# Optimization experiments

Hardware: AMD Instinct MI355X
Metric: run time of the kernel (lower is better)

The kernel has to match this reference:

```python
import jax, jax.numpy as jnp
import numpy as np

B = 32768
PASSES = 4

# mask layout: (batch, digit, row, col), values in {0,1}

def _to_lines(m, d):
    """Reorder so the last axis enumerates the 9 cells of a line and axis -2 the 9 lines."""
    if d == 'h':
        return m                      # lines = rows, cells = cols
    if d == 'v':
        return jnp.swapaxes(m, 2, 3)  # lines = cols, cells = rows
    b = m.shape[0]                    # lines = 3x3 boxes
    return m.reshape(b, 9, 3, 3, 3, 3).transpose(0, 1, 2, 4, 3, 5).reshape(b, 9, 9, 9)

_from_lines = _to_lines  # all three reorderings are self-inverse


def filter_line(m, d):
    """SudokuFilterHVBox: remove a solved cell's digit from all other cells in its line."""
    l = _to_lines(m, d)
    cnt = l.sum(axis=1, keepdims=True)                 # candidates per cell
    solved = l * (cnt == 1).astype(l.dtype)            # one-hot solved cells
    other = solved.sum(axis=-1, keepdims=True) - solved  # same digit solved elsewhere in line
    out = l * (other == 0).astype(l.dtype)
    return _from_lines(out, d)


def unique_line(m, d):
    """SudokuUniqueHVBox (hidden single): if a digit fits only one cell in a line, fix it."""
    l = _to_lines(m, d)
    cnt_line = l.sum(axis=-1, keepdims=True)           # per-digit count in the line
    hidden = l * (cnt_line == 1).astype(l.dtype)       # lone placements
    has = hidden.sum(axis=1, keepdims=True) > 0        # cell hosts a hidden single
    out = jnp.where(has, hidden, l)
    return _from_lines(out, d)


def doubles_line(m, d):
    """SudokuDigitsDoubles (naked pair): two identical 2-candidate cells in a line
    eliminate those digits from the rest of the line."""
    l = _to_lines(m, d)                                # (B, d, line, cell)
    cnt = l.sum(axis=1, keepdims=True)
    pm = l * (cnt == 2).astype(l.dtype)                # patterns of 2-candidate cells
    dot = jnp.einsum('bdlc,bdle->blce', pm, pm)        # pattern overlap between cells
    eye = jnp.eye(9, dtype=l.dtype)
    match = (dot == 2).astype(l.dtype) * (1.0 - eye)   # identical pair at another cell
    pairflag = match.sum(-1) > 0                       # (B, line, cell) part of a naked pair
    pair_digit = pm * pairflag[:, None, :, :].astype(l.dtype)
    total_pd = pair_digit.sum(-1, keepdims=True)       # digit belongs to some pair in line
    remove = (total_pd > 0) & (pair_digit == 0)
    out = l * (1.0 - remove.astype(l.dtype))
    return _from_lines(out, d)


def pointing(m, d):
    """SudokuDigitsInOneLineAtBox: if a digit's box candidates lie in one row/col,
    remove that digit from the rest of the row/col outside the box."""
    b = m.shape[0]
    v = m.reshape(b, 9, 3, 3, 3, 3)                    # (B, d, br, ri, bc, ci)
    if d == 'h':
        pres = v.sum(axis=5) > 0                       # (B,d,br,ri,bc) digit in row of box
        nrows = pres.sum(axis=3, keepdims=True)
        point = pres & (nrows == 1)                    # confined to single row within box
        tot = point.sum(axis=4, keepdims=True)         # over bc
        rem = (tot - point) > 0                        # pointing from another box hits us
        out = v * (1.0 - rem[..., None].astype(v.dtype))
    else:
        pres = v.sum(axis=3) > 0                       # (B,d,br,bc,ci) digit in col of box
        ncols = pres.sum(axis=4, keepdims=True)
        point = pres & (ncols == 1)
        tot = point.sum(axis=2, keepdims=True)         # over br
        rem = (tot - point) > 0
        out = v * (1.0 - rem[:, :, :, None, :, :].astype(v.dtype))
    return out.reshape(b, 9, 9, 9)


def _forward_mask(mask):
    for _ in range(PASSES):
        mask = filter_line(mask, 'box')
        mask = pointing(mask, 'h')
        mask = pointing(mask, 'v')
        mask = unique_line(mask, 'h')
        mask = unique_line(mask, 'v')
        mask = unique_line(mask, 'box')
        mask = doubles_line(mask, 'v')   # original code instantiates doubles_h with 'v'
        mask = doubles_line(mask, 'v')
        mask = doubles_line(mask, 'box')
    return mask


def setup_inputs() -> dict:
    key = jax.random.key(0)
    mask = jax.random.randint(key, (B, 9, 9, 9), 0, 2).astype(jnp.float32)
    return {"mask": mask}


def reference(mask):
    out = _forward_mask(mask)
    cnt = out.sum(axis=1)                              # candidates per cell
    solved = jnp.all(cnt == 1, axis=(1, 2))            # (B,) puzzle fully determined
    return (out, solved)
```

## Files before the change

### kernel.cpp

```cpp
#include <hip/hip_runtime.h>
#include <stdint.h>

#define NB 32768
#define NPASS 4
#define FULL27 0x07FFFFFFu
#define PUZ_PER_BLK 64
#define SOLVE_BLKS (NB / PUZ_PER_BLK)
#define BLK_DW 1458
#define BLK_V4 11664


__device__ __forceinline__ uint32_t colfold(uint32_t w) {
    return (w | (w >> 9) | (w >> 18)) & 0x1FFu;
}
__device__ __forceinline__ uint32_t colmaj2(uint32_t w) {
    return ((w & (w >> 9)) | ((w | (w >> 9)) & (w >> 18))) & 0x1FFu;
}
__device__ __forceinline__ uint32_t rotA(uint32_t v) {
    return (uint32_t)__builtin_amdgcn_update_dpp(0, (int)v, 0x09, 0xF, 0xF, true);
}
__device__ __forceinline__ uint32_t rotB(uint32_t v) {
    return (uint32_t)__builtin_amdgcn_update_dpp(0, (int)v, 0x12, 0xF, 0xF, true);
}
__device__ __forceinline__ uint32_t dppx1(uint32_t v) {
    return (uint32_t)__builtin_amdgcn_update_dpp(0, (int)v, 0xB1, 0xF, 0xF, true);
}
__device__ __forceinline__ uint32_t dppx2(uint32_t v) {
    return (uint32_t)__builtin_amdgcn_update_dpp(0, (int)v, 0x4E, 0xF, 0xF, true);
}

__global__ __launch_bounds__(256)
void sudoku_kernel(const uint32_t* __restrict__ in, float* __restrict__ out,
                   float* __restrict__ solved) {
    __shared__ uint32_t pool[BLK_DW + 2];
    const int tid = threadIdx.x;
    const int q = tid >> 2;
    const int band = tid & 3;
    const int P0 = blockIdx.x * PUZ_PER_BLK;

    {
        const uint4* src = (const uint4*)in + (size_t)blockIdx.x * BLK_V4;
        uint16_t* hp = (uint16_t*)pool;
        #pragma unroll 1
        for (int ii = 0; ii < 6; ++ii) {
            uint4 v[8];
            #pragma unroll
            for (int j = 0; j < 8; ++j) {
                int vi = (ii * 8 + j) * 256 + tid;
                if (vi > BLK_V4 - 1) vi = BLK_V4 - 1;
                v[j] = src[vi];
            }
            #pragma unroll
            for (int j = 0; j < 8; ++j) {
                int it = ii * 8 + j;
                uint32_t n = ((v[j].x >> 23) & 1u) | ((v[j].y >> 22) & 2u)
                           | ((v[j].z >> 21) & 4u) | ((v[j].w >> 20) & 8u);
                uint32_t b = n | (dppx1(n) << 4);
                uint32_t h = b | (dppx2(b) << 8);
                if ((tid & 3) == 0) {
                    int D = it * 32 + (tid >> 3);
                    if (D < BLK_DW)
                        hp[2 * D + ((tid >> 2) & 1)] = (uint16_t)h;
                }
            }
        }
    }
    __syncthreads();

    uint32_t bd[9];
    {
        const int bb0 = q * 729 + band * 27;
        #pragma unroll
        for (int d = 0; d < 9; ++d) {
            int bit = bb0 + d * 81;
            int di = bit >> 5, sh = bit & 31;
            uint64_t both = (uint64_t)pool[di] | ((uint64_t)pool[di + 1] << 32);
            bd[d] = (uint32_t)(both >> sh) & FULL27;
        }
    }
    __syncthreads();

    #pragma unroll 1
    for (int pass = 0; pass < NPASS; ++pass) {
        {
            uint32_t on = 0, tw = 0, fo = 0;
            #pragma unroll
            for (int d = 0; d < 9; ++d) {
                uint32_t c = on & bd[d];
                on ^= bd[d]; fo |= tw & c; tw ^= c;
            }
            uint32_t ex1 = on & ~tw & ~fo;
            #pragma unroll
            for (int d = 0; d < 9; ++d) {
                uint32_t s = bd[d] & ex1;
                #pragma unroll
                for (int k = 0; k < 3; ++k) {
                    uint32_t bm = 0x1C0E07u << (3 * k);
                    uint32_t sm = s & bm;
                    uint32_t multi = sm & (sm - 1u);
                    uint32_t keep = (sm == 0u) ? 0xFFFFFFFFu : (~bm | (multi ? 0u : sm));
                    bd[d] &= keep;
                }
            }
        }

        #pragma unroll
        for (int d = 0; d < 9; ++d) {
            uint32_t w = bd[d];
            uint32_t t = (w | (w >> 1) | (w >> 2)) & 0x01249249u;
            uint32_t sum = (t & 0x1FFu) + ((t >> 9) & 0x1FFu) + ((t >> 18) & 0x1FFu);
            uint32_t single = sum & ~(sum >> 1) & 0x49u;
            uint32_t point = t & (single * 0x40201u);
            uint32_t clearm = 0;
            #pragma unroll
            for (int r = 0; r < 3; ++r) {
                uint32_t pr = (point >> (9 * r)) & 0x1FFu;
                uint32_t multi = pr & (pr - 1u);
                uint32_t segkeep = multi ? 0u : pr * 7u;
                uint32_t rc = pr ? ((0x1FFu & ~segkeep) << (9 * r)) : 0u;
                clearm |= rc;
            }
            bd[d] = w & ~clearm;
        }

        {
            uint32_t pnt[9];
            #pragma unroll
            for (int d = 0; d < 9; ++d) {
                uint32_t w = bd[d];
                uint32_t qq = colfold(w);
                uint32_t u = (qq & 0x49u) + ((qq >> 1) & 0x49u) + ((qq >> 2) & 0x49u);
                uint32_t single = u & ~(u >> 1) & 0x49u;
                pnt[d] = qq & (single * 7u);
            }
            #pragma unroll
            for (int d = 0; d < 9; ++d) {
                uint32_t o = rotA(pnt[d]) | rotB(pnt[d]);
                bd[d] &= ~(o * 0x40201u);
            }
        }

        {
            uint32_t hid[9], has = 0;
            #pragma unroll
            for (int d = 0; d < 9; ++d) {
                uint32_t w = bd[d], h = 0;
                #pragma unroll
                for (int r = 0; r < 3; ++r) {
                    uint32_t x = w & (0x1FFu << (9 * r));
                    h |= (x & (x - 1u)) ? 0u : x;
                }
                hid[d] = h; has |= h;
            }
            #pragma unroll
            for (int d = 0; d < 9; ++d) bd[d] = (bd[d] & ~has) | hid[d];
        }

        {
            uint32_t hid[9], has = 0;
            #pragma unroll
            for (int d = 0; d < 9; ++d) {
                uint32_t w = bd[d];
                uint32_t q0 = colfold(w), m0 = colmaj2(w);
                uint32_t ex = q0 | (m0 << 9);
                uint32_t ea = rotA(ex);
                uint32_t eb = rotB(ex);
                uint32_t qa = ea & 0x1FFu, ma = ea >> 9;
                uint32_t qb = eb & 0x1FFu, mb = eb >> 9;
                uint32_t ge2 = m0 | ma | mb | (q0 & qa) | (q0 & qb) | (qa & qb);
                uint32_t ex1c = (q0 | qa | qb) & ~ge2;
                hid[d] = w & ((ex1c & q0) * 0x40201u);
                has |= hid[d];
            }
            #pragma unroll
            for (int d = 0; d < 9; ++d) bd[d] = (bd[d] & ~has) | hid[d];
        }

        {
            uint32_t hid[9], has = 0;
            #pragma unroll
            for (int d = 0; d < 9; ++d) {
                uint32_t w = bd[d], h = 0;
                #pragma unroll
                for (int k = 0; k < 3; ++k) {
                    uint32_t x = w & (0x1C0E07u << (3 * k));
                    h |= (x & (x - 1u)) ? 0u : x;
                }
                hid[d] = h; has |= h;
            }
            #pragma unroll
            for (int d = 0; d < 9; ++d) bd[d] = (bd[d] & ~has) | hid[d];
        }

        #pragma unroll 1
        for (int rep = 0; rep < 2; ++rep) {
            uint32_t on = 0, tw = 0, fo = 0;
            #pragma unroll
            for (int d = 0; d < 9; ++d) {
                uint32_t c = on & bd[d];
                on ^= bd[d]; fo |= tw & c; tw ^= c;
            }
            uint32_t ex2 = tw & ~on & ~fo;
            uint32_t Q[9], K[9];
            #pragma unroll
            for (int d = 0; d < 9; ++d) { Q[d] = bd[d] & ex2; K[d] = 0u; }
            #pragma unroll
            for (int d1 = 0; d1 < 9; ++d1)
                #pragma unroll
                for (int d2 = d1 + 1; d2 < 9; ++d2) {
                    uint32_t P = Q[d1] & Q[d2];
                    uint32_t f0 = colfold(P), g0 = colmaj2(P);
                    uint32_t ex = f0 | (g0 << 9);
                    uint32_t ea = rotA(ex);
                    uint32_t eb = rotB(ex);
                    uint32_t fa = ea & 0x1FFu, ga = ea >> 9;
                    uint32_t fb = eb & 0x1FFu, gb = eb >> 9;
                    uint32_t dup = g0 | ga | gb | (f0 & fa) | (f0 & fb) | (fa & fb);
                    uint32_t sK = P & (dup * 0x40201u);
                    K[d1] |= sK; K[d2] |= sK;
                }
            #pragma unroll
            for (int d = 0; d < 9; ++d) {
                uint32_t kc = colfold(K[d]);
                uint32_t cols = kc | rotA(kc) | rotB(kc);
                uint32_t em = cols * 0x40201u;
                bd[d] = (bd[d] & ~em) | K[d];
            }
        }

        {
            uint32_t on = 0, tw = 0, fo = 0;
            #pragma unroll
            for (int d = 0; d < 9; ++d) {
                uint32_t c = on & bd[d];
                on ^= bd[d]; fo |= tw & c; tw ^= c;
            }
            uint32_t ex2 = tw & ~on & ~fo;
            uint32_t Q[9], K[9];
            #pragma unroll
            for (int d = 0; d < 9; ++d) { Q[d] = bd[d] & ex2; K[d] = 0u; }
            #pragma unroll
            for (int d1 = 0; d1 < 9; ++d1)
                #pragma unroll
                for (int d2 = d1 + 1; d2 < 9; ++d2) {
                    uint32_t P = Q[d1] & Q[d2];
                    #pragma unroll
                    for (int k = 0; k < 3; ++k) {
                        uint32_t m = P & (0x1C0E07u << (3 * k));
                        uint32_t s = (m & (m - 1u)) ? m : 0u;
                        K[d1] |= s; K[d2] |= s;
                    }
                }
            #pragma unroll
            for (int d = 0; d < 9; ++d)
                #pragma unroll
                for (int k = 0; k < 3; ++k) {
                    uint32_t bm = 0x1C0E07u << (3 * k);
                    uint32_t t = K[d] & bm;
                    uint32_t mask = t ? (~bm | t) : 0xFFFFFFFFu;
                    bd[d] &= mask;
                }
        }
    }

    {
        uint32_t on = 0, tw = 0, fo = 0;
        #pragma unroll
        for (int d = 0; d < 9; ++d) {
            uint32_t c = on & bd[d];
            on ^= bd[d]; fo |= tw & c; tw ^= c;
        }
        uint32_t okb = ((on & ~tw & ~fo) == FULL27) ? 1u : 0u;
        uint32_t all = okb & rotA(okb) & rotB(okb);
        if (band == 0) solved[P0 + q] = all ? 1.0f : 0.0f;
    }

    for (int j = tid; j < BLK_DW + 2; j += 256) pool[j] = 0u;
    __syncthreads();
    if (band != 3) {
        const int pbit = q * 729;
        #pragma unroll
        for (int d = 0; d < 9; ++d) {
            int bitbase = pbit + d * 81 + band * 27;
            int di = bitbase >> 5;
            int sh = bitbase & 31;
            uint64_t both = (uint64_t)bd[d] << sh;
            atomicOr(&pool[di], (uint32_t)both);
            atomicOr(&pool[di + 1], (uint32_t)(both >> 32));
        }
    }
    __syncthreads();
    {
        float4* dst4 = (float4*)(out + (size_t)P0 * 729);
        #pragma unroll 4
        for (int i = 0; i < 46; ++i) {
            int j = i * 256 + tid;
            if (j < 11664) {
                uint32_t nib = (pool[j >> 3] >> ((j & 7) * 4)) & 0xFu;
                dst4[j] = make_float4((float)(nib & 1u), (float)((nib >> 1) & 1u),
                                      (float)((nib >> 2) & 1u), (float)((nib >> 3) & 1u));
            }
        }
    }
}

extern "C" void kernel_launch(void* const* d_in, const int* in_sizes, int n_in,
                              void* d_out, int out_size, void* d_ws, size_t ws_size,
                              hipStream_t stream) {
    const uint32_t* in = (const uint32_t*)d_in[0];
    float* out = (float*)d_out;
    float* solved = out + (size_t)NB * 729;
    sudoku_kernel<<<SOLVE_BLKS, 256, 0, stream>>>(in, out, solved);
}
```

Before: 215.6 us.

## Stream input via async global-to-LDS loads with triple-buffered staging

Replaces the register-batched global loads of the float mask with direct global_load_lds transfers into a three-slot LDS staging ring, keeping two chunks in flight while the current chunk is packed into bits. Manual vmcnt waits and a sched barrier order the pipeline. Launch bounds now request two blocks per CU to raise occupancy. The change adds about 48KB of LDS per block, which may limit residency, and depends on raw waitcnt semantics to be correct.

```diff
diff --git a/kernel.cpp b/kernel.cpp
--- a/kernel.cpp
+++ b/kernel.cpp
@@ -8,6 +8,7 @@
 #define SOLVE_BLKS (NB / PUZ_PER_BLK)
 #define BLK_DW 1458
 #define BLK_V4 11664
+#define NCHUNK 12
 
 
 __device__ __forceinline__ uint32_t colfold(uint32_t w) {
@@ -29,41 +30,56 @@
     return (uint32_t)__builtin_amdgcn_update_dpp(0, (int)v, 0x4E, 0xF, 0xF, true);
 }
 
-__global__ __launch_bounds__(256)
+__global__ __launch_bounds__(256, 2)
 void sudoku_kernel(const uint32_t* __restrict__ in, float* __restrict__ out,
                    float* __restrict__ solved) {
     __shared__ uint32_t pool[BLK_DW + 2];
+    __shared__ uint4 stage[3][1024];
     const int tid = threadIdx.x;
     const int q = tid >> 2;
     const int band = tid & 3;
+    const int w = tid >> 6;
+    const int lane = tid & 63;
     const int P0 = blockIdx.x * PUZ_PER_BLK;
 
     {
-        const uint4* src = (const uint4*)in + (size_t)blockIdx.x * BLK_V4;
+        const uint4* src4 = (const uint4*)in + (size_t)blockIdx.x * BLK_V4;
         uint16_t* hp = (uint16_t*)pool;
-        #pragma unroll 1
-        for (int ii = 0; ii < 6; ++ii) {
-            uint4 v[8];
-            #pragma unroll
-            for (int j = 0; j < 8; ++j) {
-                int vi = (ii * 8 + j) * 256 + tid;
-                if (vi > BLK_V4 - 1) vi = BLK_V4 - 1;
-                v[j] = src[vi];
-            }
-            #pragma unroll
-            for (int j = 0; j < 8; ++j) {
-                int it = ii * 8 + j;
-                uint32_t n = ((v[j].x >> 23) & 1u) | ((v[j].y >> 22) & 2u)
-                           | ((v[j].z >> 21) & 4u) | ((v[j].w >> 20) & 8u);
+
+        #define ISSUE(c)                                                          \
+            { _Pragma("unroll")                                                   \
+              for (int i = 0; i < 4; ++i) {                                       \
+                  int g = (c) * 1024 + w * 256 + i * 64 + lane;                   \
+                  if (g > BLK_V4 - 1) g = BLK_V4 - 1;                             \
+                  __builtin_amdgcn_global_load_lds(                               \
+                      (const __attribute__((address_space(1))) void*)(src4 + g),  \
+                      (__attribute__((address_space(3))) void*)                   \
+                          &stage[(c) % 3][w * 256 + i * 64],                      \
+                      16, 0, 0);                                                  \
+              } }
+
+        ISSUE(0);
+        ISSUE(1);
+        #pragma unroll
+        for (int c = 0; c < NCHUNK; ++c) {
+            if (c < NCHUNK - 1) asm volatile("s_waitcnt vmcnt(4)" ::: "memory");
+            else                asm volatile("s_waitcnt vmcnt(0)" ::: "memory");
+            __builtin_amdgcn_sched_barrier(0);
+            #pragma unroll
+            for (int j = 0; j < 4; ++j) {
+                uint4 v = stage[c % 3][w * 256 + j * 64 + lane];
+                uint32_t n = ((v.x >> 23) & 1u) | ((v.y >> 22) & 2u)
+                           | ((v.z >> 21) & 4u) | ((v.w >> 20) & 8u);
                 uint32_t b = n | (dppx1(n) << 4);
                 uint32_t h = b | (dppx2(b) << 8);
-                if ((tid & 3) == 0) {
-                    int D = it * 32 + (tid >> 3);
-                    if (D < BLK_DW)
-                        hp[2 * D + ((tid >> 2) & 1)] = (uint16_t)h;
-                }
-            }
-        }
+                if ((lane & 3) == 0) {
+                    int t = (c * 1024 + w * 256 + j * 64 + lane) >> 2;
+                    if (t < 2 * BLK_DW) hp[t] = (uint16_t)h;
+                }
+            }
+            if (c < NCHUNK - 2) ISSUE(c + 2);
+        }
+        #undef ISSUE
     }
     __syncthreads();
 
@@ -106,8 +122,8 @@
 
         #pragma unroll
         for (int d = 0; d < 9; ++d) {
-            uint32_t w = bd[d];
-            uint32_t t = (w | (w >> 1) | (w >> 2)) & 0x01249249u;
+            uint32_t ww = bd[d];
+            uint32_t t = (ww | (ww >> 1) | (ww >> 2)) & 0x01249249u;
             uint32_t sum = (t & 0x1FFu) + ((t >> 9) & 0x1FFu) + ((t >> 18) & 0x1FFu);
             uint32_t single = sum & ~(sum >> 1) & 0x49u;
             uint32_t point = t & (single * 0x40201u);
@@ -120,15 +136,15 @@
                 uint32_t rc = pr ? ((0x1FFu & ~segkeep) << (9 * r)) : 0u;
                 clearm |= rc;
             }
-            bd[d] = w & ~clearm;
+            bd[d] = ww & ~clearm;
         }
 
         {
             uint32_t pnt[9];
             #pragma unroll
             for (int d = 0; d < 9; ++d) {
-                uint32_t w = bd[d];
-                uint32_t qq = colfold(w);
+                uint32_t ww = bd[d];
+                uint32_t qq = colfold(ww);
                 uint32_t u = (qq & 0x49u) + ((qq >> 1) & 0x49u) + ((qq >> 2) & 0x49u);
                 uint32_t single = u & ~(u >> 1) & 0x49u;
                 pnt[d] = qq & (single * 7u);
@@ -144,10 +160,10 @@
             uint32_t hid[9], has = 0;
             #pragma unroll
             for (int d = 0; d < 9; ++d) {
-                uint32_t w = bd[d], h = 0;
+                uint32_t ww = bd[d], h = 0;
                 #pragma unroll
                 for (int r = 0; r < 3; ++r) {
-                    uint32_t x = w & (0x1FFu << (9 * r));
+                    uint32_t x = ww & (0x1FFu << (9 * r));
                     h |= (x & (x - 1u)) ? 0u : x;
                 }
                 hid[d] = h; has |= h;
@@ -160,8 +176,8 @@
             uint32_t hid[9], has = 0;
             #pragma unroll
             for (int d = 0; d < 9; ++d) {
-                uint32_t w = bd[d];
-                uint32_t q0 = colfold(w), m0 = colmaj2(w);
+                uint32_t ww = bd[d];
+                uint32_t q0 = colfold(ww), m0 = colmaj2(ww);
                 uint32_t ex = q0 | (m0 << 9);
                 uint32_t ea = rotA(ex);
                 uint32_t eb = rotB(ex);
@@ -169,7 +185,7 @@
                 uint32_t qb = eb & 0x1FFu, mb = eb >> 9;
                 uint32_t ge2 = m0 | ma | mb | (q0 & qa) | (q0 & qb) | (qa & qb);
                 uint32_t ex1c = (q0 | qa | qb) & ~ge2;
-                hid[d] = w & ((ex1c & q0) * 0x40201u);
+                hid[d] = ww & ((ex1c & q0) * 0x40201u);
                 has |= hid[d];
             }
             #pragma unroll
@@ -180,10 +196,10 @@
             uint32_t hid[9], has = 0;
             #pragma unroll
             for (int d = 0; d < 9; ++d) {
-                uint32_t w = bd[d], h = 0;
+                uint32_t ww = bd[d], h = 0;
                 #pragma unroll
                 for (int k = 0; k < 3; ++k) {
-                    uint32_t x = w & (0x1C0E07u << (3 * k));
+                    uint32_t x = ww & (0x1C0E07u << (3 * k));
                     h |= (x & (x - 1u)) ? 0u : x;
                 }
                 hid[d] = h; has |= h;
```

Result: no change. 213.4 us (-1.0%).

## Shrink blocks to one wavefront of 16 puzzles and replace multiplies with shifts

Applied to the files above, without the earlier changes.

Each block now handles 16 puzzles with a single 64-lane wavefront instead of 64 puzzles with 256 threads. The load and store loops are rewritten for that size, and the per-block shared pool shrinks to match. Constant multiplies used to broadcast bit fields are replaced by shift-or helpers. The smaller blocks aim to cut barrier cost, since __syncthreads covers only one wave, and to raise the number of resident blocks. The cost is more blocks and a serial load loop with one outstanding 16-byte load per lane per iteration instead of eight batched loads.

```diff
diff --git a/kernel.cpp b/kernel.cpp
--- a/kernel.cpp
+++ b/kernel.cpp
@@ -4,10 +4,10 @@
 #define NB 32768
 #define NPASS 4
 #define FULL27 0x07FFFFFFu
-#define PUZ_PER_BLK 64
-#define SOLVE_BLKS (NB / PUZ_PER_BLK)
-#define BLK_DW 1458
-#define BLK_V4 11664
+#define PPW 16
+#define NBLK (NB / PPW)
+#define POOL_DW 368
+#define BLK_V4 2916
 
 
 __device__ __forceinline__ uint32_t colfold(uint32_t w) {
@@ -16,6 +16,12 @@
 __device__ __forceinline__ uint32_t colmaj2(uint32_t w) {
     return ((w & (w >> 9)) | ((w | (w >> 9)) & (w >> 18))) & 0x1FFu;
 }
+__device__ __forceinline__ uint32_t bcast3(uint32_t x) {
+    return x | (x << 9) | (x << 18);
+}
+__device__ __forceinline__ uint32_t mul7s(uint32_t x) {
+    return x | (x << 1) | (x << 2);
+}
 __device__ __forceinline__ uint32_t rotA(uint32_t v) {
     return (uint32_t)__builtin_amdgcn_update_dpp(0, (int)v, 0x09, 0xF, 0xF, true);
 }
@@ -29,39 +35,30 @@
     return (uint32_t)__builtin_amdgcn_update_dpp(0, (int)v, 0x4E, 0xF, 0xF, true);
 }
 
-__global__ __launch_bounds__(256)
+__global__ __launch_bounds__(64)
 void sudoku_kernel(const uint32_t* __restrict__ in, float* __restrict__ out,
                    float* __restrict__ solved) {
-    __shared__ uint32_t pool[BLK_DW + 2];
-    const int tid = threadIdx.x;
-    const int q = tid >> 2;
-    const int band = tid & 3;
-    const int P0 = blockIdx.x * PUZ_PER_BLK;
+    __shared__ uint32_t pool[POOL_DW];
+    const int lane = threadIdx.x;
+    const int q = lane >> 2;
+    const int band = lane & 3;
+    const int P0 = blockIdx.x * PPW;
 
     {
-        const uint4* src = (const uint4*)in + (size_t)blockIdx.x * BLK_V4;
+        const uint4* src4 = (const uint4*)in + (size_t)blockIdx.x * BLK_V4;
         uint16_t* hp = (uint16_t*)pool;
         #pragma unroll 1
-        for (int ii = 0; ii < 6; ++ii) {
-            uint4 v[8];
-            #pragma unroll
-            for (int j = 0; j < 8; ++j) {
-                int vi = (ii * 8 + j) * 256 + tid;
-                if (vi > BLK_V4 - 1) vi = BLK_V4 - 1;
-                v[j] = src[vi];
-            }
-            #pragma unroll
-            for (int j = 0; j < 8; ++j) {
-                int it = ii * 8 + j;
-                uint32_t n = ((v[j].x >> 23) & 1u) | ((v[j].y >> 22) & 2u)
-                           | ((v[j].z >> 21) & 4u) | ((v[j].w >> 20) & 8u);
-                uint32_t b = n | (dppx1(n) << 4);
-                uint32_t h = b | (dppx2(b) << 8);
-                if ((tid & 3) == 0) {
-                    int D = it * 32 + (tid >> 3);
-                    if (D < BLK_DW)
-                        hp[2 * D + ((tid >> 2) & 1)] = (uint16_t)h;
-                }
+        for (int i = 0; i < 46; ++i) {
+            int g = i * 64 + lane;
+            int gc = g > BLK_V4 - 1 ? BLK_V4 - 1 : g;
+            uint4 v = src4[gc];
+            uint32_t n = ((v.x >> 23) & 1u) | ((v.y >> 22) & 2u)
+                       | ((v.z >> 21) & 4u) | ((v.w >> 20) & 8u);
+            uint32_t b = n | (dppx1(n) << 4);
+            uint32_t h = b | (dppx2(b) << 8);
+            if ((lane & 3) == 0) {
+                int t = g >> 2;
+                if (t < 730) hp[t] = (uint16_t)h;
             }
         }
     }
@@ -110,13 +107,13 @@
             uint32_t t = (w | (w >> 1) | (w >> 2)) & 0x01249249u;
             uint32_t sum = (t & 0x1FFu) + ((t >> 9) & 0x1FFu) + ((t >> 18) & 0x1FFu);
             uint32_t single = sum & ~(sum >> 1) & 0x49u;
-            uint32_t point = t & (single * 0x40201u);
+            uint32_t point = t & bcast3(single);
             uint32_t clearm = 0;
             #pragma unroll
             for (int r = 0; r < 3; ++r) {
                 uint32_t pr = (point >> (9 * r)) & 0x1FFu;
                 uint32_t multi = pr & (pr - 1u);
-                uint32_t segkeep = multi ? 0u : pr * 7u;
+                uint32_t segkeep = multi ? 0u : mul7s(pr);
                 uint32_t rc = pr ? ((0x1FFu & ~segkeep) << (9 * r)) : 0u;
                 clearm |= rc;
             }
@@ -131,12 +128,12 @@
                 uint32_t qq = colfold(w);
                 uint32_t u = (qq & 0x49u) + ((qq >> 1) & 0x49u) + ((qq >> 2) & 0x49u);
                 uint32_t single = u & ~(u >> 1) & 0x49u;
-                pnt[d] = qq & (single * 7u);
+                pnt[d] = qq & mul7s(single);
             }
             #pragma unroll
             for (int d = 0; d < 9; ++d) {
                 uint32_t o = rotA(pnt[d]) | rotB(pnt[d]);
-                bd[d] &= ~(o * 0x40201u);
+                bd[d] &= ~bcast3(o);
             }
         }
 
@@ -169,7 +166,7 @@
                 uint32_t qb = eb & 0x1FFu, mb = eb >> 9;
                 uint32_t ge2 = m0 | ma | mb | (q0 & qa) | (q0 & qb) | (qa & qb);
                 uint32_t ex1c = (q0 | qa | qb) & ~ge2;
-                hid[d] = w & ((ex1c & q0) * 0x40201u);
+                hid[d] = w & bcast3(ex1c & q0);
                 has |= hid[d];
             }
             #pragma unroll
@@ -216,14 +213,14 @@
                     uint32_t fa = ea & 0x1FFu, ga = ea >> 9;
                     uint32_t fb = eb & 0x1FFu, gb = eb >> 9;
                     uint32_t dup = g0 | ga | gb | (f0 & fa) | (f0 & fb) | (fa & fb);
-                    uint32_t sK = P & (dup * 0x40201u);
+                    uint32_t sK = P & bcast3(dup);
                     K[d1] |= sK; K[d2] |= sK;
                 }
             #pragma unroll
             for (int d = 0; d < 9; ++d) {
                 uint32_t kc = colfold(K[d]);
                 uint32_t cols = kc | rotA(kc) | rotB(kc);
-                uint32_t em = cols * 0x40201u;
+                uint32_t em = bcast3(cols);
                 bd[d] = (bd[d] & ~em) | K[d];
             }
         }
@@ -275,7 +272,11 @@
         if (band == 0) solved[P0 + q] = all ? 1.0f : 0.0f;
     }
 
-    for (int j = tid; j < BLK_DW + 2; j += 256) pool[j] = 0u;
+    #pragma unroll
+    for (int i = 0; i < 6; ++i) {
+        int j = i * 64 + lane;
+        if (j < POOL_DW) pool[j] = 0u;
+    }
     __syncthreads();
     if (band != 3) {
         const int pbit = q * 729;
@@ -294,8 +295,8 @@
         float4* dst4 = (float4*)(out + (size_t)P0 * 729);
         #pragma unroll 4
         for (int i = 0; i < 46; ++i) {
-            int j = i * 256 + tid;
-            if (j < 11664) {
+            int j = i * 64 + lane;
+            if (j < BLK_V4) {
                 uint32_t nib = (pool[j >> 3] >> ((j & 7) * 4)) & 0xFu;
                 dst4[j] = make_float4((float)(nib & 1u), (float)((nib >> 1) & 1u),
                                       (float)((nib >> 2) & 1u), (float)((nib >> 3) & 1u));
@@ -310,5 +311,5 @@
     const uint32_t* in = (const uint32_t*)d_in[0];
     float* out = (float*)d_out;
     float* solved = out + (size_t)NB * 729;
-    sudoku_kernel<<<SOLVE_BLKS, 256, 0, stream>>>(in, out, solved);
-}
+    sudoku_kernel<<<NBLK, 64, 0, stream>>>(in, out, solved);
+}
```

Result: slower. 223.5 us (+3.7%).
